# Performance work log

Hardware: AMD Instinct MI355X
Metric: run time of the kernel (lower is better)

## Reference

```python
import jax, jax.numpy as jnp
import numpy as np

LN_EPS = 1e-5

def setup_inputs() -> dict:
    key = jax.random.key(0)
    ks = jax.random.split(key, 9)
    B, N, D, E, H = 1, 50000, 128, 800000, 8
    s = 1.0 / np.sqrt(D)
    x = jax.random.normal(ks[0], (B, N, D), jnp.float32)
    edge_index = jax.random.randint(ks[1], (2, E), 0, N, dtype=jnp.int64)
    edge_weights = jax.random.uniform(ks[2], (E,), jnp.float32)
    Wq = jax.random.normal(ks[3], (D, D), jnp.float32) * s
    Wk = jax.random.normal(ks[4], (D, D), jnp.float32) * s
    Wv = jax.random.normal(ks[5], (D, D), jnp.float32) * s
    We = jax.random.normal(ks[6], (H, 1), jnp.float32)  # edge_encoder: Linear(1, H, bias=False)
    Wo = jax.random.normal(ks[7], (D, D), jnp.float32) * s
    gamma = jnp.ones((D,), jnp.float32)
    beta = jnp.zeros((D,), jnp.float32)
    return {"x": x, "edge_index": edge_index, "edge_weights": edge_weights,
            "Wq": Wq, "Wk": Wk, "Wv": Wv, "We": We, "Wo": Wo,
            "gamma": gamma, "beta": beta}


def reference(x, edge_index, edge_weights, Wq, Wk, Wv, We, Wo, gamma, beta):
    B, N, D = x.shape
    H = We.shape[0]
    d = D // H
    scale = 1.0 / np.sqrt(d)

    # QKV projections -> [B, N, H, d]
    Q = (x @ Wq.T).reshape(B, N, H, d)
    K = (x @ Wk.T).reshape(B, N, H, d)
    V = (x @ Wv.T).reshape(B, N, H, d)

    src, dst = edge_index[0], edge_index[1]

    # Edge-indexed gathers: [B, E, H, d]
    Qe = Q[:, src]
    Ke = K[:, dst]
    Ve = V[:, dst]

    # Per-edge scores [B, E, H] + edge bias (Linear(1,H) on edge_weights)
    scores = jnp.einsum('behd,behd->beh', Qe, Ke) * scale
    scores = scores + (edge_weights[:, None] * We[None, :, 0])[None]  # [1,E,H]

    # Segment (scatter) softmax over src neighborhoods, segment axis first: [E, B, H]
    s = jnp.moveaxis(scores, 1, 0)
    m = jax.ops.segment_max(s, src, num_segments=N)          # [N, B, H]
    e = jnp.exp(s - m[src])
    denom = jax.ops.segment_sum(e, src, num_segments=N)      # [N, B, H]
    attn = e / denom[src]                                    # [E, B, H]

    # Weighted scatter-add aggregation: [N, B, H, d]
    wV = attn[..., None] * jnp.moveaxis(Ve, 1, 0)
    agg = jax.ops.segment_sum(wV, src, num_segments=N)

    attn_out = jnp.moveaxis(agg, 0, 1).reshape(B, N, D)
    out = attn_out @ Wo.T

    # Residual + LayerNorm
    y = x + out
    mu = y.mean(-1, keepdims=True)
    var = ((y - mu) ** 2).mean(-1, keepdims=True)
    return (y - mu) / jnp.sqrt(var + LN_EPS) * gamma + beta
```

## Files before the change

### kernel.cpp

```cpp
#include <hip/hip_runtime.h>
#include <hip/hip_bf16.h>
#include <math.h>


#define CAP  64
#define NBIN 256
#define CAPB 4096

typedef __attribute__((ext_vector_type(8))) short short8;
typedef __attribute__((ext_vector_type(4))) float f32x4;
typedef __attribute__((ext_vector_type(4))) int i32x4;

static __device__ __forceinline__ ushort f2bf(float f) {
  unsigned u = __float_as_uint(f);
  u += 0x7fff + ((u >> 16) & 1);
  return (ushort)(u >> 16);
}
static __device__ __forceinline__ float bflo(unsigned u) {
  return __uint_as_float(u << 16);
}
static __device__ __forceinline__ float bfhi(unsigned u) {
  return __uint_as_float(u & 0xffff0000u);
}

__global__ __launch_bounds__(256) void prep_kernel(
    const float* __restrict__ Wq, const float* __restrict__ Wk,
    const float* __restrict__ Wv, const float* __restrict__ Wo,
    ushort* __restrict__ Wb) {
  int tid = blockIdx.x * 256 + threadIdx.x;
  if (tid < 16384) {
    int i = tid * 4;
    const float* src = (i < 16384) ? Wq : (i < 32768) ? Wk : (i < 49152) ? Wv : Wo;
    int off = i & 16383;
    float4 v = *(const float4*)(src + off);
    *(ushort4*)(Wb + i) = make_ushort4(f2bf(v.x), f2bf(v.y), f2bf(v.z), f2bf(v.w));
  }
}

__global__ __launch_bounds__(256) void qkv_binA_kernel(
    const float* __restrict__ x, const ushort* __restrict__ Wb,
    float* __restrict__ Qf, ushort* __restrict__ KVb,
    const int* __restrict__ ei, const float* __restrict__ ew,
    int* __restrict__ binCnt, uint2* __restrict__ binArr,
    int N, int E, int QB) {
  __shared__ int  lcnt[NBIN];
  __shared__ int  loff[NBIN];
  __shared__ int  lpos[NBIN];
  __shared__ int  gbase[NBIN];
  __shared__ uint2 stage[2048];

  if ((int)blockIdx.x >= QB) {
    int sb = (int)blockIdx.x - QB;
    int t  = threadIdx.x;
    int e0 = sb * 2048 + t * 8;
    int nblk = min(2048, E - sb * 2048);
    if (nblk < 0) nblk = 0;

    lcnt[t] = 0;
    __syncthreads();

    int ss[8], dd[8]; float ww[8]; int bn[8];
    bool val[8];
#pragma unroll
    for (int i = 0; i < 8; i++) {
      int e = e0 + i;
      val[i] = e < E;
      if (val[i]) { ss[i] = ei[e]; dd[i] = ei[E + e]; ww[i] = ew[e]; }
      else        { ss[i] = 0; dd[i] = 0; ww[i] = 0.f; }
      bn[i] = (int)((long)ss[i] * NBIN / N);
      if (val[i]) atomicAdd(&lcnt[bn[i]], 1);
    }
    __syncthreads();

    if (t == 0) {
      int a = 0;
      for (int b = 0; b < NBIN; b++) { int c = lcnt[b]; loff[b] = a; lpos[b] = a; a += c; }
    }
    __syncthreads();

#pragma unroll
    for (int i = 0; i < 8; i++) {
      if (val[i]) {
        int p = atomicAdd(&lpos[bn[i]], 1);
        stage[p] = make_uint2(((unsigned)ss[i] << 15) | ((unsigned)f2bf(ww[i]) & 0x7fffu),
                              (unsigned)dd[i]);
      }
    }
    __syncthreads();

    gbase[t] = (lcnt[t] > 0) ? atomicAdd(&binCnt[t], lcnt[t]) : 0;
    __syncthreads();

    for (int i = t; i < nblk; i += 256) {
      uint2 rec = stage[i];
      int s = (int)(rec.x >> 15);
      int b = (int)((long)s * NBIN / N);
      int pos = gbase[b] + (i - loff[b]);
      if (pos < CAPB) binArr[(size_t)b * CAPB + pos] = rec;
    }
    return;
  }

  int bid = (int)blockIdx.x;
  int m = bid % 3, t = bid / 3;
  int w = threadIdx.x >> 6, l = threadIdx.x & 63;
  int n0 = t * 256 + w * 64;
  int lr = l & 15, lg = l >> 4;

  short8 a[4][4];
#pragma unroll
  for (int rt = 0; rt < 4; rt++) {
    int arow = n0 + rt * 16 + lr;
    if (arow < N) {
      const float* xrow = x + (size_t)arow * 128 + 8 * lg;
      float4 x0[4], x1[4];
#pragma unroll
      for (int ks = 0; ks < 4; ks++) {
        x0[ks] = *(const float4*)(xrow + 32 * ks);
        x1[ks] = *(const float4*)(xrow + 32 * ks + 4);
      }
#pragma unroll
      for (int ks = 0; ks < 4; ks++) {
        short8 tt;
        tt[0] = f2bf(x0[ks].x); tt[1] = f2bf(x0[ks].y); tt[2] = f2bf(x0[ks].z); tt[3] = f2bf(x0[ks].w);
        tt[4] = f2bf(x1[ks].x); tt[5] = f2bf(x1[ks].y); tt[6] = f2bf(x1[ks].z); tt[7] = f2bf(x1[ks].w);
        a[rt][ks] = tt;
      }
    } else {
#pragma unroll
      for (int ks = 0; ks < 4; ks++) a[rt][ks] = (short8){0,0,0,0,0,0,0,0};
    }
  }

  const ushort* Wm = Wb + m * 16384;
#pragma unroll
  for (int ctp = 0; ctp < 4; ctp++) {
    short8 b[2][4];
#pragma unroll
    for (int ci = 0; ci < 2; ci++) {
      const ushort* wrow = Wm + (size_t)((ctp * 2 + ci) * 16 + lr) * 128 + 8 * lg;
#pragma unroll
      for (int ks = 0; ks < 4; ks++) b[ci][ks] = *(const short8*)(wrow + 32 * ks);
    }
#pragma unroll
    for (int rt = 0; rt < 4; rt++) {
#pragma unroll
      for (int ci = 0; ci < 2; ci++) {
        f32x4 acc = {0.f, 0.f, 0.f, 0.f};
#pragma unroll
        for (int ks = 0; ks < 4; ks++)
          acc = __builtin_amdgcn_mfma_f32_16x16x32_bf16(a[rt][ks], b[ci][ks], acc, 0, 0, 0);
        int c = (ctp * 2 + ci) * 16 + lr;
#pragma unroll
        for (int r = 0; r < 4; r++) {
          int row = n0 + rt * 16 + 4 * lg + r;
          if (row < N) {
            if (m == 0)      Qf[(size_t)row * 128 + c] = acc[r];
            else if (m == 1) KVb[(size_t)row * 256 + c] = f2bf(acc[r]);
            else             KVb[(size_t)row * 256 + 128 + c] = f2bf(acc[r]);
          }
        }
      }
    }
  }
}

__global__ __launch_bounds__(256) void passB_kernel(
    const int* __restrict__ binCnt, const uint2* __restrict__ binArr,
    int* __restrict__ cnt, unsigned* __restrict__ recs, int N, int E) {
  int b = blockIdx.x;
  int nb = min(binCnt[b], CAPB);
  const uint2* arr = binArr + (size_t)b * CAPB;
  for (int i = threadIdx.x; i < nb; i += 256) {
    uint2 rec = arr[i];
    int s = (int)(rec.x >> 15);
    int r = atomicAdd(&cnt[s], 1);
    if (r < CAP) recs[((size_t)s << 6) + r] = (rec.y << 15) | (rec.x & 0x7fffu);
  }
}

__global__ __launch_bounds__(256) void edge_attn_kernel(
    const float* __restrict__ Qf, const ushort* __restrict__ KVb,
    const unsigned* __restrict__ recs, const float* __restrict__ We,
    const int* __restrict__ cnt, ushort* __restrict__ AGGb, int N) {
  int wv = threadIdx.x >> 6, l = threadIdx.x & 63;
  int n = blockIdx.x * 4 + wv;
  if (n >= N) return;
  int u = l >> 3, h = l & 7;
  int deg = min(cnt[n], CAP);
  ushort* op = AGGb + (size_t)n * 128 + (h << 4);

  if (deg <= 0) {
    if (u == 0) {
      *(uint4*)(op + 0) = make_uint4(0, 0, 0, 0);
      *(uint4*)(op + 8) = make_uint4(0, 0, 0, 0);
    }
    return;
  }

  const unsigned* rb = recs + ((size_t)n << 6);
  unsigned myrec = rb[min(l, deg - 1)];

  float q[16];
  const float* qp = Qf + (size_t)n * 128 + (h << 4);
  *(float4*)(q + 0)  = *(const float4*)(qp + 0);
  *(float4*)(q + 4)  = *(const float4*)(qp + 4);
  *(float4*)(q + 8)  = *(const float4*)(qp + 8);
  *(float4*)(q + 12) = *(const float4*)(qp + 12);
  float weh = We[h];

  float m = -INFINITY, de = 0.f;
  float acc[16];
#pragma unroll
  for (int d = 0; d < 16; d++) acc[d] = 0.f;

  for (int base = 0; base < deg; base += 8) {
    int idx = base + u;
    unsigned rec = __shfl(myrec, idx);
    const ushort* kv = KVb + (((rec >> 15) << 8) + (h << 4));
    uint4 k0 = *(const uint4*)kv;
    uint4 k1 = *(const uint4*)(kv + 8);
    uint4 v0 = *(const uint4*)(kv + 128);
    uint4 v1 = *(const uint4*)(kv + 136);

    float s;
    s  = q[0]  * bflo(k0.x) + q[1]  * bfhi(k0.x);
    s += q[2]  * bflo(k0.y) + q[3]  * bfhi(k0.y);
    s += q[4]  * bflo(k0.z) + q[5]  * bfhi(k0.z);
    s += q[6]  * bflo(k0.w) + q[7]  * bfhi(k0.w);
    s += q[8]  * bflo(k1.x) + q[9]  * bfhi(k1.x);
    s += q[10] * bflo(k1.y) + q[11] * bfhi(k1.y);
    s += q[12] * bflo(k1.z) + q[13] * bfhi(k1.z);
    s += q[14] * bflo(k1.w) + q[15] * bfhi(k1.w);
    s = s * 0.25f + __uint_as_float((rec & 0x7fffu) << 16) * weh;
    if (idx >= deg) s = -INFINITY;

    float p;
    if (s > m + 8.f) {
      float c = __expf(m - s);
      de *= c;
#pragma unroll
      for (int d = 0; d < 16; d++) acc[d] *= c;
      m = s;
      p = 1.f;
    } else {
      p = __expf(s - m);
    }
    de += p;
    acc[0]  += p * bflo(v0.x); acc[1]  += p * bfhi(v0.x);
    acc[2]  += p * bflo(v0.y); acc[3]  += p * bfhi(v0.y);
    acc[4]  += p * bflo(v0.z); acc[5]  += p * bfhi(v0.z);
    acc[6]  += p * bflo(v0.w); acc[7]  += p * bfhi(v0.w);
    acc[8]  += p * bflo(v1.x); acc[9]  += p * bfhi(v1.x);
    acc[10] += p * bflo(v1.y); acc[11] += p * bfhi(v1.y);
    acc[12] += p * bflo(v1.z); acc[13] += p * bfhi(v1.z);
    acc[14] += p * bflo(v1.w); acc[15] += p * bfhi(v1.w);
  }

  bool live = (m > -INFINITY);
  if (!live) {
    de = 0.f;
#pragma unroll
    for (int d = 0; d < 16; d++) acc[d] = 0.f;
  }
  float M = m;
  M = fmaxf(M, __shfl_xor(M, 8));
  M = fmaxf(M, __shfl_xor(M, 16));
  M = fmaxf(M, __shfl_xor(M, 32));
  float c = live ? __expf(m - M) : 0.f;
  de *= c;
#pragma unroll
  for (int d = 0; d < 16; d++) acc[d] *= c;
  de += __shfl_xor(de, 8); de += __shfl_xor(de, 16); de += __shfl_xor(de, 32);
#pragma unroll
  for (int d = 0; d < 16; d++) {
    acc[d] += __shfl_xor(acc[d], 8);
    acc[d] += __shfl_xor(acc[d], 16);
    acc[d] += __shfl_xor(acc[d], 32);
  }

  if (u == 0) {
    float inv = (de > 0.f) ? 1.0f / de : 0.f;
    unsigned o[8];
#pragma unroll
    for (int j = 0; j < 8; j++) {
      ushort lo = f2bf(acc[2 * j] * inv);
      ushort hi = f2bf(acc[2 * j + 1] * inv);
      o[j] = (unsigned)lo | ((unsigned)hi << 16);
    }
    *(uint4*)(op + 0) = make_uint4(o[0], o[1], o[2], o[3]);
    *(uint4*)(op + 8) = make_uint4(o[4], o[5], o[6], o[7]);
  }
}

__global__ __launch_bounds__(256) void wo_ln_kernel(
    const ushort* __restrict__ AGGb, const ushort* __restrict__ Wob,
    const float* __restrict__ x, const float* __restrict__ gamma,
    const float* __restrict__ beta, float* __restrict__ out, int N) {
  int w = threadIdx.x >> 6, l = threadIdx.x & 63;
  int n0 = blockIdx.x * 128 + w * 32;
  int lr = l & 15, lg = l >> 4;

  short8 a[2][4];
#pragma unroll
  for (int rt = 0; rt < 2; rt++) {
    int arow = n0 + rt * 16 + lr;
    if (arow < N) {
      const ushort* ap = AGGb + (size_t)arow * 128 + 8 * lg;
#pragma unroll
      for (int ks = 0; ks < 4; ks++) a[rt][ks] = *(const short8*)(ap + 32 * ks);
    } else {
#pragma unroll
      for (int ks = 0; ks < 4; ks++) a[rt][ks] = (short8){0,0,0,0,0,0,0,0};
    }
  }

  f32x4 acc[2][8];
#pragma unroll
  for (int ctp = 0; ctp < 4; ctp++) {
    short8 b[2][4];
#pragma unroll
    for (int ci = 0; ci < 2; ci++) {
      const ushort* wrow = Wob + (size_t)((ctp * 2 + ci) * 16 + lr) * 128 + 8 * lg;
#pragma unroll
      for (int ks = 0; ks < 4; ks++) b[ci][ks] = *(const short8*)(wrow + 32 * ks);
    }
#pragma unroll
    for (int rt = 0; rt < 2; rt++)
#pragma unroll
      for (int ci = 0; ci < 2; ci++) {
        int ct = ctp * 2 + ci;
        acc[rt][ct] = (f32x4){0.f, 0.f, 0.f, 0.f};
#pragma unroll
        for (int ks = 0; ks < 4; ks++)
          acc[rt][ct] = __builtin_amdgcn_mfma_f32_16x16x32_bf16(a[rt][ks], b[ci][ks], acc[rt][ct], 0, 0, 0);
      }
  }
  float g[8], bt[8];
#pragma unroll
  for (int ct = 0; ct < 8; ct++) { g[ct] = gamma[ct * 16 + lr]; bt[ct] = beta[ct * 16 + lr]; }

#pragma unroll
  for (int rt = 0; rt < 2; rt++) {
#pragma unroll
    for (int r = 0; r < 4; r++) {
      int row = n0 + rt * 16 + 4 * lg + r;
      bool ok = row < N;
      float v[8], s = 0.f, s2 = 0.f;
#pragma unroll
      for (int ct = 0; ct < 8; ct++) {
        float xv = ok ? x[(size_t)row * 128 + ct * 16 + lr] : 0.f;
        v[ct] = acc[rt][ct][r] + xv;
        s += v[ct]; s2 += v[ct] * v[ct];
      }
#pragma unroll
      for (int d = 1; d < 16; d <<= 1) { s += __shfl_xor(s, d); s2 += __shfl_xor(s2, d); }
      float mu = s * (1.f / 128.f);
      float var = s2 * (1.f / 128.f) - mu * mu;
      float rs = rsqrtf(var + 1e-5f);
      if (ok) {
#pragma unroll
        for (int ct = 0; ct < 8; ct++)
          out[(size_t)row * 128 + ct * 16 + lr] = (v[ct] - mu) * rs * g[ct] + bt[ct];
      }
    }
  }
}

extern "C" void kernel_launch(void* const* d_in, const int* in_sizes, int n_in,
                              void* d_out, int out_size, void* d_ws, size_t ws_size,
                              hipStream_t stream) {
  const float* x     = (const float*)d_in[0];
  const int*   ei    = (const int*)d_in[1];
  const float* ew    = (const float*)d_in[2];
  const float* Wq    = (const float*)d_in[3];
  const float* Wk    = (const float*)d_in[4];
  const float* Wv    = (const float*)d_in[5];
  const float* We    = (const float*)d_in[6];
  const float* Wo    = (const float*)d_in[7];
  const float* gamma = (const float*)d_in[8];
  const float* beta  = (const float*)d_in[9];

  int N = in_sizes[0] / 128;
  int E = in_sizes[1] / 2;
  int Npad = (N + 255) & ~255;
  int QB = 3 * (Npad / 256);
  int BA = (E + 2047) / 2048;

  char* ws = (char*)d_ws;
  ushort* Wb   = (ushort*)ws; ws += 4 * 16384 * 2;
  float*  Qf   = (float*)ws;  ws += (size_t)Npad * 128 * 4;
  ushort* KVb  = (ushort*)ws; ws += (size_t)Npad * 256 * 2;
  ushort* AGGb = (ushort*)ws; ws += (size_t)Npad * 128 * 2;
  int* cnt  = (int*)ws; ws += (size_t)N * 4;
  unsigned* recs = (unsigned*)ws; ws += (size_t)N * CAP * 4;
  int* binCnt = (int*)ws; ws += (size_t)NBIN * 4;
  uint2* binArr = (uint2*)ws; ws += (size_t)NBIN * CAPB * 8;
  ushort* Wob = Wb + 3 * 16384;

  hipMemsetAsync(cnt, 0, (size_t)N * 4, stream);
  hipMemsetAsync(binCnt, 0, (size_t)NBIN * 4, stream);

  prep_kernel<<<64, 256, 0, stream>>>(Wq, Wk, Wv, Wo, Wb);

  qkv_binA_kernel<<<QB + BA, 256, 0, stream>>>(x, Wb, Qf, KVb, ei, ew, binCnt, binArr, N, E, QB);

  passB_kernel<<<NBIN, 256, 0, stream>>>(binCnt, binArr, cnt, recs, N, E);

  edge_attn_kernel<<<(N + 3) / 4, 256, 0, stream>>>(Qf, KVb, recs, We, cnt, AGGb, N);

  wo_ln_kernel<<<Npad / 128, 256, 0, stream>>>(AGGb, Wob, x, gamma, beta, (float*)d_out, N);
}
```

Before: 146.3 us.

## Store Q/K/V as fp16, use fdot2 scores, process two edges per iteration

```diff
diff --git a/kernel.cpp b/kernel.cpp
--- a/kernel.cpp
+++ b/kernel.cpp
@@ -9,18 +9,26 @@
 
 typedef __attribute__((ext_vector_type(8))) short short8;
 typedef __attribute__((ext_vector_type(4))) float f32x4;
-typedef __attribute__((ext_vector_type(4))) int i32x4;
+typedef _Float16 h2 __attribute__((ext_vector_type(2)));
 
 static __device__ __forceinline__ ushort f2bf(float f) {
   unsigned u = __float_as_uint(f);
   u += 0x7fff + ((u >> 16) & 1);
   return (ushort)(u >> 16);
 }
-static __device__ __forceinline__ float bflo(unsigned u) {
-  return __uint_as_float(u << 16);
-}
-static __device__ __forceinline__ float bfhi(unsigned u) {
-  return __uint_as_float(u & 0xffff0000u);
+static __device__ __forceinline__ ushort f2h(float f) {
+  _Float16 h = (_Float16)f;
+  ushort u; __builtin_memcpy(&u, &h, 2); return u;
+}
+static __device__ __forceinline__ h2 u2h2(unsigned u) {
+  h2 v; __builtin_memcpy(&v, &u, 4); return v;
+}
+static __device__ __forceinline__ float dot2(h2 a, h2 b, float c) {
+#if __has_builtin(__builtin_amdgcn_fdot2)
+  return __builtin_amdgcn_fdot2(a, b, c, false);
+#else
+  return c + (float)a[0] * (float)b[0] + (float)a[1] * (float)b[1];
+#endif
 }
 
 __global__ __launch_bounds__(256) void prep_kernel(
@@ -39,7 +47,7 @@
 
 __global__ __launch_bounds__(256) void qkv_binA_kernel(
     const float* __restrict__ x, const ushort* __restrict__ Wb,
-    float* __restrict__ Qf, ushort* __restrict__ KVb,
+    ushort* __restrict__ Qh, ushort* __restrict__ KVb,
     const int* __restrict__ ei, const float* __restrict__ ew,
     int* __restrict__ binCnt, uint2* __restrict__ binArr,
     int N, int E, int QB) {
@@ -155,9 +163,9 @@
         for (int r = 0; r < 4; r++) {
           int row = n0 + rt * 16 + 4 * lg + r;
           if (row < N) {
-            if (m == 0)      Qf[(size_t)row * 128 + c] = acc[r];
-            else if (m == 1) KVb[(size_t)row * 256 + c] = f2bf(acc[r]);
-            else             KVb[(size_t)row * 256 + 128 + c] = f2bf(acc[r]);
+            if (m == 0)      Qh[(size_t)row * 128 + c] = f2h(acc[r]);
+            else if (m == 1) KVb[(size_t)row * 256 + c] = f2h(acc[r]);
+            else             KVb[(size_t)row * 256 + 128 + c] = f2h(acc[r]);
           }
         }
       }
@@ -180,7 +188,7 @@
 }
 
 __global__ __launch_bounds__(256) void edge_attn_kernel(
-    const float* __restrict__ Qf, const ushort* __restrict__ KVb,
+    const ushort* __restrict__ Qh, const ushort* __restrict__ KVb,
     const unsigned* __restrict__ recs, const float* __restrict__ We,
     const int* __restrict__ cnt, ushort* __restrict__ AGGb, int N) {
   int wv = threadIdx.x >> 6, l = threadIdx.x & 63;
@@ -201,12 +209,14 @@
   const unsigned* rb = recs + ((size_t)n << 6);
   unsigned myrec = rb[min(l, deg - 1)];
 
-  float q[16];
-  const float* qp = Qf + (size_t)n * 128 + (h << 4);
-  *(float4*)(q + 0)  = *(const float4*)(qp + 0);
-  *(float4*)(q + 4)  = *(const float4*)(qp + 4);
-  *(float4*)(q + 8)  = *(const float4*)(qp + 8);
-  *(float4*)(q + 12) = *(const float4*)(qp + 12);
+  h2 q2[8];
+  {
+    const ushort* qp = Qh + (size_t)n * 128 + (h << 4);
+    uint4 qa = *(const uint4*)qp;
+    uint4 qb = *(const uint4*)(qp + 8);
+    q2[0] = u2h2(qa.x); q2[1] = u2h2(qa.y); q2[2] = u2h2(qa.z); q2[3] = u2h2(qa.w);
+    q2[4] = u2h2(qb.x); q2[5] = u2h2(qb.y); q2[6] = u2h2(qb.z); q2[7] = u2h2(qb.w);
+  }
   float weh = We[h];
 
   float m = -INFINITY, de = 0.f;
@@ -214,47 +224,79 @@
 #pragma unroll
   for (int d = 0; d < 16; d++) acc[d] = 0.f;
 
-  for (int base = 0; base < deg; base += 8) {
-    int idx = base + u;
-    unsigned rec = __shfl(myrec, idx);
-    const ushort* kv = KVb + (((rec >> 15) << 8) + (h << 4));
-    uint4 k0 = *(const uint4*)kv;
-    uint4 k1 = *(const uint4*)(kv + 8);
-    uint4 v0 = *(const uint4*)(kv + 128);
-    uint4 v1 = *(const uint4*)(kv + 136);
-
-    float s;
-    s  = q[0]  * bflo(k0.x) + q[1]  * bfhi(k0.x);
-    s += q[2]  * bflo(k0.y) + q[3]  * bfhi(k0.y);
-    s += q[4]  * bflo(k0.z) + q[5]  * bfhi(k0.z);
-    s += q[6]  * bflo(k0.w) + q[7]  * bfhi(k0.w);
-    s += q[8]  * bflo(k1.x) + q[9]  * bfhi(k1.x);
-    s += q[10] * bflo(k1.y) + q[11] * bfhi(k1.y);
-    s += q[12] * bflo(k1.z) + q[13] * bfhi(k1.z);
-    s += q[14] * bflo(k1.w) + q[15] * bfhi(k1.w);
-    s = s * 0.25f + __uint_as_float((rec & 0x7fffu) << 16) * weh;
-    if (idx >= deg) s = -INFINITY;
-
-    float p;
-    if (s > m + 8.f) {
-      float c = __expf(m - s);
-      de *= c;
-#pragma unroll
-      for (int d = 0; d < 16; d++) acc[d] *= c;
-      m = s;
-      p = 1.f;
-    } else {
-      p = __expf(s - m);
-    }
-    de += p;
-    acc[0]  += p * bflo(v0.x); acc[1]  += p * bfhi(v0.x);
-    acc[2]  += p * bflo(v0.y); acc[3]  += p * bfhi(v0.y);
-    acc[4]  += p * bflo(v0.z); acc[5]  += p * bfhi(v0.z);
-    acc[6]  += p * bflo(v0.w); acc[7]  += p * bfhi(v0.w);
-    acc[8]  += p * bflo(v1.x); acc[9]  += p * bfhi(v1.x);
-    acc[10] += p * bflo(v1.y); acc[11] += p * bfhi(v1.y);
-    acc[12] += p * bflo(v1.z); acc[13] += p * bfhi(v1.z);
-    acc[14] += p * bflo(v1.w); acc[15] += p * bfhi(v1.w);
+  for (int base = 0; base < deg; base += 16) {
+    int idx0 = base + u, idx1 = base + 8 + u;
+    unsigned rec0 = __shfl(myrec, idx0);
+    unsigned rec1 = __shfl(myrec, idx1 < CAP ? idx1 : CAP - 1);
+    const ushort* kv0 = KVb + (((rec0 >> 15) << 8) + (h << 4));
+    const ushort* kv1 = KVb + (((rec1 >> 15) << 8) + (h << 4));
+    uint4 k0a = *(const uint4*)kv0;
+    uint4 k0b = *(const uint4*)(kv0 + 8);
+    uint4 v0a = *(const uint4*)(kv0 + 128);
+    uint4 v0b = *(const uint4*)(kv0 + 136);
+    uint4 k1a = *(const uint4*)kv1;
+    uint4 k1b = *(const uint4*)(kv1 + 8);
+    uint4 v1a = *(const uint4*)(kv1 + 128);
+    uint4 v1b = *(const uint4*)(kv1 + 136);
+
+    float s0 = 0.f, s1 = 0.f;
+    s0 = dot2(q2[0], u2h2(k0a.x), s0); s0 = dot2(q2[1], u2h2(k0a.y), s0);
+    s0 = dot2(q2[2], u2h2(k0a.z), s0); s0 = dot2(q2[3], u2h2(k0a.w), s0);
+    s0 = dot2(q2[4], u2h2(k0b.x), s0); s0 = dot2(q2[5], u2h2(k0b.y), s0);
+    s0 = dot2(q2[6], u2h2(k0b.z), s0); s0 = dot2(q2[7], u2h2(k0b.w), s0);
+    s1 = dot2(q2[0], u2h2(k1a.x), s1); s1 = dot2(q2[1], u2h2(k1a.y), s1);
+    s1 = dot2(q2[2], u2h2(k1a.z), s1); s1 = dot2(q2[3], u2h2(k1a.w), s1);
+    s1 = dot2(q2[4], u2h2(k1b.x), s1); s1 = dot2(q2[5], u2h2(k1b.y), s1);
+    s1 = dot2(q2[6], u2h2(k1b.z), s1); s1 = dot2(q2[7], u2h2(k1b.w), s1);
+    s0 = s0 * 0.25f + __uint_as_float((rec0 & 0x7fffu) << 16) * weh;
+    s1 = s1 * 0.25f + __uint_as_float((rec1 & 0x7fffu) << 16) * weh;
+    if (idx0 >= deg) s0 = -INFINITY;
+    if (idx1 >= deg) s1 = -INFINITY;
+
+    {
+      float p;
+      if (s0 > m + 8.f) {
+        float c = __expf(m - s0);
+        de *= c;
+#pragma unroll
+        for (int d = 0; d < 16; d++) acc[d] *= c;
+        m = s0; p = 1.f;
+      } else {
+        p = __expf(s0 - m);
+      }
+      de += p;
+      h2 t;
+      t = u2h2(v0a.x); acc[0]  += p * (float)t[0]; acc[1]  += p * (float)t[1];
+      t = u2h2(v0a.y); acc[2]  += p * (float)t[0]; acc[3]  += p * (float)t[1];
+      t = u2h2(v0a.z); acc[4]  += p * (float)t[0]; acc[5]  += p * (float)t[1];
+      t = u2h2(v0a.w); acc[6]  += p * (float)t[0]; acc[7]  += p * (float)t[1];
+      t = u2h2(v0b.x); acc[8]  += p * (float)t[0]; acc[9]  += p * (float)t[1];
+      t = u2h2(v0b.y); acc[10] += p * (float)t[0]; acc[11] += p * (float)t[1];
+      t = u2h2(v0b.z); acc[12] += p * (float)t[0]; acc[13] += p * (float)t[1];
+      t = u2h2(v0b.w); acc[14] += p * (float)t[0]; acc[15] += p * (float)t[1];
+    }
+    {
+      float p;
+      if (s1 > m + 8.f) {
+        float c = __expf(m - s1);
+        de *= c;
+#pragma unroll
+        for (int d = 0; d < 16; d++) acc[d] *= c;
+        m = s1; p = 1.f;
+      } else {
+        p = __expf(s1 - m);
+      }
+      de += p;
+      h2 t;
+      t = u2h2(v1a.x); acc[0]  += p * (float)t[0]; acc[1]  += p * (float)t[1];
+      t = u2h2(v1a.y); acc[2]  += p * (float)t[0]; acc[3]  += p * (float)t[1];
+      t = u2h2(v1a.z); acc[4]  += p * (float)t[0]; acc[5]  += p * (float)t[1];
+      t = u2h2(v1a.w); acc[6]  += p * (float)t[0]; acc[7]  += p * (float)t[1];
+      t = u2h2(v1b.x); acc[8]  += p * (float)t[0]; acc[9]  += p * (float)t[1];
+      t = u2h2(v1b.y); acc[10] += p * (float)t[0]; acc[11] += p * (float)t[1];
+      t = u2h2(v1b.z); acc[12] += p * (float)t[0]; acc[13] += p * (float)t[1];
+      t = u2h2(v1b.w); acc[14] += p * (float)t[0]; acc[15] += p * (float)t[1];
+    }
   }
 
   bool live = (m > -INFINITY);
@@ -389,7 +431,7 @@
 
   char* ws = (char*)d_ws;
   ushort* Wb   = (ushort*)ws; ws += 4 * 16384 * 2;
-  float*  Qf   = (float*)ws;  ws += (size_t)Npad * 128 * 4;
+  ushort* Qh   = (ushort*)ws; ws += (size_t)Npad * 128 * 2;
   ushort* KVb  = (ushort*)ws; ws += (size_t)Npad * 256 * 2;
   ushort* AGGb = (ushort*)ws; ws += (size_t)Npad * 128 * 2;
   int* cnt  = (int*)ws; ws += (size_t)N * 4;
@@ -403,11 +445,11 @@
 
   prep_kernel<<<64, 256, 0, stream>>>(Wq, Wk, Wv, Wo, Wb);
 
-  qkv_binA_kernel<<<QB + BA, 256, 0, stream>>>(x, Wb, Qf, KVb, ei, ew, binCnt, binArr, N, E, QB);
+  qkv_binA_kernel<<<QB + BA, 256, 0, stream>>>(x, Wb, Qh, KVb, ei, ew, binCnt, binArr, N, E, QB);
 
   passB_kernel<<<NBIN, 256, 0, stream>>>(binCnt, binArr, cnt, recs, N, E);
 
-  edge_attn_kernel<<<(N + 3) / 4, 256, 0, stream>>>(Qf, KVb, recs, We, cnt, AGGb, N);
+  edge_attn_kernel<<<(N + 3) / 4, 256, 0, stream>>>(Qh, KVb, recs, We, cnt, AGGb, N);
 
   wo_ln_kernel<<<Npad / 128, 256, 0, stream>>>(AGGb, Wob, x, gamma, beta, (float*)d_out, N);
 }
```

Measured after the change: 145.4 us. Within noise of the previous version (-0.6%).
